# Performance work log

Hardware: AMD Instinct MI355X
Metric: run time of the kernel (lower is better)

Reference implementation:

```python
import jax, jax.numpy as jnp
import numpy as np


def _bicubic_warp(img, dx, dy):
    """Faithful JAX port of Warp_Object.forward with flag='bicubic'.
    img: [B,C,H,W] float32; dx, dy: [B,1,H,W] pixel displacements.
    Replicates the original tile-order quirk: X/Y are repeated C times along
    dim0 (order c*B+b) while the image is flattened in b*C+c order.
    """
    B, C, H, W = img.shape
    Wm1 = jnp.float32(max(W - 1, 1))
    Hm1 = jnp.float32(max(H - 1, 1))
    xs = jnp.arange(W, dtype=jnp.float32)
    ys = jnp.arange(H, dtype=jnp.float32)
    Xg, Yg = jnp.meshgrid(xs, ys)          # [H,W]
    # normalized grid in [-1,1] as in forward()
    newX = 2.0 * (Xg[None] + dx[:, 0]) / Wm1 - 1.0   # [B,H,W]
    newY = 2.0 * (Yg[None] + dy[:, 0]) / Hm1 - 1.0
    # repeat over channels exactly like X.repeat([C,1,1,1]) (tile order)
    x_map = (jnp.tile(newX, (C, 1, 1)) + 1.0) * Wm1 / 2.0   # [B*C,H,W]
    y_map = (jnp.tile(newY, (C, 1, 1)) + 1.0) * Hm1 / 2.0

    x0 = jnp.floor(x_map)
    y0 = jnp.floor(y_map)
    tx = x_map - x0
    ty = y_map - y0

    def cubic_coeffs(t):
        cm1 = (-t ** 3 + 2.0 * t ** 2 - t) / 2.0
        c0 = (3.0 * t ** 3 - 5.0 * t ** 2 + 2.0) / 2.0
        c1 = (-3.0 * t ** 3 + 4.0 * t ** 2 + t) / 2.0
        c2 = 1.0 - (cm1 + c0 + c1)
        return (cm1, c0, c1, c2)

    cx = cubic_coeffs(tx)
    cy = cubic_coeffs(ty)

    x0i = x0.astype(jnp.int32)
    y0i = y0.astype(jnp.int32)
    xi = [jnp.clip(x0i + o, 0, W - 1) for o in (-1, 0, 1, 2)]
    yi = [jnp.clip(y0i + o, 0, H - 1) for o in (-1, 0, 1, 2)]

    flat = img.reshape(B * C, H, W)
    row = jnp.arange(B * C)[:, None, None]   # per-image base offset

    out = jnp.zeros_like(x_map)
    for j in range(4):            # 4 rows of the 4x4 bicubic stencil
        row_acc = jnp.zeros_like(x_map)
        for i in range(4):
            row_acc = row_acc + cx[i] * flat[row, yi[j], xi[i]]
        out = out + cy[j] * row_acc
    return out.reshape(B, C, H, W)


def setup_inputs() -> dict:
    key = jax.random.key(0)
    k1, k2, k3 = jax.random.split(key, 3)
    B, C, H, W = 4, 3, 512, 512
    input_image = jax.random.normal(k1, (B, C, H, W), dtype=jnp.float32)
    delta_x = jax.random.normal(k2, (B, 1, H, W), dtype=jnp.float32) * 1.5
    delta_y = jax.random.normal(k3, (B, 1, H, W), dtype=jnp.float32) * 1.5
    return {"input_image": input_image, "delta_x": delta_x, "delta_y": delta_y}


def reference(input_image, delta_x, delta_y):
    return _bicubic_warp(input_image, delta_x, delta_y)
```

## Files before the change

### kernel.cpp

```cpp
#include <hip/hip_runtime.h>


constexpr int B = 4, C = 3, H = 512, W = 512;
constexpr int HW = H * W;
constexpr int TH = 4;
constexpr int HALO_UP = 6, HALO_DN = 7;
constexpr int RS = TH + HALO_UP + HALO_DN;
constexpr int LST = 272;
constexpr int NPOS = 2;
constexpr int NT = 512;
constexpr int NB = B * (H / TH) * 2;

typedef float f4 __attribute__((ext_vector_type(4)));
typedef f4 f4u __attribute__((aligned(4)));

__global__ __launch_bounds__(NT, 8)
void warp_bicubic_xsplit(const float* __restrict__ img,
                         const float* __restrict__ dxp,
                         const float* __restrict__ dyp,
                         float* __restrict__ out)
{
    __shared__ float tile[RS * LST];

    int b   = blockIdx.x;
    int swz = (b & 7) * (NB / 8) + (b >> 3);
    int bd   = swz >> 8;
    int band = (swz >> 1) & 127;
    int half = swz & 1;
    int yb   = band * TH;
    int xb   = half * 256;
    int cb   = half ? 248 : 0;

    int tid  = threadIdx.x;
    int wave = tid >> 6;
    int ry   = wave >> 1;
    int hw   = wave & 1;
    int lane = tid & 63;
    int y    = yb + ry;
    int xs   = xb + hw * 128 + lane;
    int pixoff = y * W + xs;

    float dxa[NPOS], dya[NPOS];
#pragma unroll
    for (int p = 0; p < NPOS; ++p) {
        dxa[p] = __builtin_nontemporal_load(dxp + bd * HW + pixoff + 64 * p);
        dya[p] = __builtin_nontemporal_load(dyp + bd * HW + pixoff + 64 * p);
    }

    float wx[NPOS][4];
    float cyw[NPOS][4];
    unsigned relv[NPOS];
    unsigned lsv[NPOS];
#pragma unroll
    for (int p = 0; p < NPOS; ++p) {
        int x = xs + 64 * p;
        float xm = (float)x + dxa[p];
        float ym = (float)y + dya[p];
        float x0f = floorf(xm), y0f = floorf(ym);
        float tx = xm - x0f, ty = ym - y0f;
        int x0 = (int)x0f, y0 = (int)y0f;
        int s  = min(max(x0 - 1, 0), W - 4);

        float tx2 = tx * tx, tx3 = tx2 * tx;
        float cx0 = (-tx3 + 2.0f * tx2 - tx) * 0.5f;
        float cx1 = (3.0f * tx3 - 5.0f * tx2 + 2.0f) * 0.5f;
        float cx2 = (-3.0f * tx3 + 4.0f * tx2 + tx) * 0.5f;
        float cx3 = 1.0f - (cx0 + cx1 + cx2);

        float ty2 = ty * ty, ty3 = ty2 * ty;
        cyw[p][0] = (-ty3 + 2.0f * ty2 - ty) * 0.5f;
        cyw[p][1] = (3.0f * ty3 - 5.0f * ty2 + 2.0f) * 0.5f;
        cyw[p][2] = (-3.0f * ty3 + 4.0f * ty2 + ty) * 0.5f;
        cyw[p][3] = 1.0f - (cyw[p][0] + cyw[p][1] + cyw[p][2]);

        if (__builtin_expect(x0 >= 1 && x0 <= W - 3, 1)) {
            wx[p][0] = cx0; wx[p][1] = cx1; wx[p][2] = cx2; wx[p][3] = cx3;
        } else {
            float w0 = 0.f, w1 = 0.f, w2 = 0.f, w3 = 0.f;
            const float cxa[4] = {cx0, cx1, cx2, cx3};
#pragma unroll
            for (int o = 0; o < 4; ++o) {
                int xi = min(max(x0 - 1 + o, 0), W - 1);
                int e  = xi - s;
                float c = cxa[o];
                w0 += (e == 0) ? c : 0.f;
                w1 += (e == 1) ? c : 0.f;
                w2 += (e == 2) ? c : 0.f;
                w3 += (e == 3) ? c : 0.f;
            }
            wx[p][0] = w0; wx[p][1] = w1; wx[p][2] = w2; wx[p][3] = w3;
        }

        relv[p] = (unsigned)(y0 - (yb - HALO_UP + 1));
        lsv[p]  = (unsigned)(s - cb);
    }

#pragma unroll
    for (int c = 0; c < C; ++c) {
        int kp = bd + 4 * c;
        const float* __restrict__ plane = img + (size_t)kp * HW;

        if (c > 0) __syncthreads();
        for (int cc = tid; cc < RS * (LST / 4); cc += NT) {
            int r   = cc / (LST / 4);
            int c4  = (cc - r * (LST / 4)) * 4;
            int scol = min(cb + c4, W - 4);
            int sr   = min(max(yb - HALO_UP + r, 0), H - 1);
            *(f4*)&tile[r * LST + c4] = *(const f4*)(plane + sr * W + scol);
        }
        __syncthreads();

        float* __restrict__ obase = out + (size_t)kp * HW + pixoff;
#pragma unroll
        for (int p = 0; p < NPOS; ++p) {
            float acc;
            if (__builtin_expect(relv[p] <= (unsigned)(RS - 4) &&
                                 lsv[p]  <= (unsigned)(LST - 4), 1)) {
                const float* rp = &tile[relv[p] * LST + lsv[p]];
                float r0 = cyw[p][0] * (wx[p][0]*rp[0] + wx[p][1]*rp[1] + wx[p][2]*rp[2] + wx[p][3]*rp[3]);
                rp += LST;
                float r1 = cyw[p][1] * (wx[p][0]*rp[0] + wx[p][1]*rp[1] + wx[p][2]*rp[2] + wx[p][3]*rp[3]);
                rp += LST;
                float r2 = cyw[p][2] * (wx[p][0]*rp[0] + wx[p][1]*rp[1] + wx[p][2]*rp[2] + wx[p][3]*rp[3]);
                rp += LST;
                float r3 = cyw[p][3] * (wx[p][0]*rp[0] + wx[p][1]*rp[1] + wx[p][2]*rp[2] + wx[p][3]*rp[3]);
                acc = (r0 + r1) + (r2 + r3);
            } else {
                int y0 = (int)relv[p] + (yb - HALO_UP + 1);
                int s  = (int)lsv[p] + cb;
                acc = 0.f;
#pragma unroll
                for (int j = 0; j < 4; ++j) {
                    int yi = min(max(y0 - 1 + j, 0), H - 1);
                    f4 v = *(const f4u*)(plane + yi * W + s);
                    acc += cyw[p][j] * (wx[p][0]*v.x + wx[p][1]*v.y + wx[p][2]*v.z + wx[p][3]*v.w);
                }
            }
            __builtin_nontemporal_store(acc, obase + 64 * p);
        }
    }
}

extern "C" void kernel_launch(void* const* d_in, const int* in_sizes, int n_in,
                              void* d_out, int out_size, void* d_ws, size_t ws_size,
                              hipStream_t stream) {
    const float* img = (const float*)d_in[0];
    const float* dx  = (const float*)d_in[1];
    const float* dy  = (const float*)d_in[2];
    float* out = (float*)d_out;

    dim3 block(NT);
    dim3 grid(NB);
    hipLaunchKernelGGL(warp_bicubic_xsplit, grid, block, 0, stream,
                       img, dx, dy, out);
}
```

Baseline: 17.65 us.

## Double-buffer channel tiles with async global-to-LDS loads and taller bands

Replaces the per-channel load-then-compute tile staging with a double-buffered LDS scheme. It uses global_load_lds to prefetch the next channel's tile while the current channel is interpolated. The band height doubles to 8 rows and the block grows to 1024 threads, which cuts the relative halo overhead and halves the block count. The in-tile test and LDS base offset are also precomputed once per pixel. In exchange the kernel uses twice the LDS per block and relies on correct waitcnt and barrier ordering for the asynchronous LDS writes, and larger blocks may reduce scheduling flexibility.

```diff
diff --git a/kernel.cpp b/kernel.cpp
--- a/kernel.cpp
+++ b/kernel.cpp
@@ -3,29 +3,38 @@
 
 constexpr int B = 4, C = 3, H = 512, W = 512;
 constexpr int HW = H * W;
-constexpr int TH = 4;
+constexpr int TH = 8;
 constexpr int HALO_UP = 6, HALO_DN = 7;
 constexpr int RS = TH + HALO_UP + HALO_DN;
 constexpr int LST = 272;
+constexpr int CH_ROW = LST / 4;
+constexpr int NCHUNK = RS * CH_ROW;
 constexpr int NPOS = 2;
-constexpr int NT = 512;
+constexpr int NT = 1024;
 constexpr int NB = B * (H / TH) * 2;
 
 typedef float f4 __attribute__((ext_vector_type(4)));
 typedef f4 f4u __attribute__((aligned(4)));
 
+typedef const __attribute__((address_space(1))) void* gas_t;
+typedef __attribute__((address_space(3))) void* las_t;
+
+__device__ __forceinline__ void gload_lds16(const float* g, float* l) {
+    __builtin_amdgcn_global_load_lds((gas_t)g, (las_t)l, 16, 0, 0);
+}
+
 __global__ __launch_bounds__(NT, 8)
-void warp_bicubic_xsplit(const float* __restrict__ img,
-                         const float* __restrict__ dxp,
-                         const float* __restrict__ dyp,
-                         float* __restrict__ out)
+void warp_bicubic_dbuf(const float* __restrict__ img,
+                       const float* __restrict__ dxp,
+                       const float* __restrict__ dyp,
+                       float* __restrict__ out)
 {
-    __shared__ float tile[RS * LST];
+    __shared__ float tile[2][RS * LST];
 
     int b   = blockIdx.x;
     int swz = (b & 7) * (NB / 8) + (b >> 3);
-    int bd   = swz >> 8;
-    int band = (swz >> 1) & 127;
+    int bd   = swz >> 7;
+    int band = (swz >> 1) & 63;
     int half = swz & 1;
     int yb   = band * TH;
     int xb   = half * 256;
@@ -40,6 +49,17 @@
     int xs   = xb + hw * 128 + lane;
     int pixoff = y * W + xs;
 
+    {
+        const float* plane = img + (size_t)bd * HW;
+        for (int cc = tid; cc < NCHUNK; cc += NT) {
+            int r  = cc / CH_ROW;
+            int c4 = (cc - r * CH_ROW) * 4;
+            int scol = min(cb + c4, W - 4);
+            int sr   = min(max(yb - HALO_UP + r, 0), H - 1);
+            gload_lds16(plane + sr * W + scol, &tile[0][cc * 4]);
+        }
+    }
+
     float dxa[NPOS], dya[NPOS];
 #pragma unroll
     for (int p = 0; p < NPOS; ++p) {
@@ -49,8 +69,9 @@
 
     float wx[NPOS][4];
     float cyw[NPOS][4];
-    unsigned relv[NPOS];
-    unsigned lsv[NPOS];
+    int   lbase[NPOS];
+    unsigned relv[NPOS], lsv[NPOS];
+    bool  intile[NPOS];
 #pragma unroll
     for (int p = 0; p < NPOS; ++p) {
         int x = xs + 64 * p;
@@ -91,32 +112,37 @@
             wx[p][0] = w0; wx[p][1] = w1; wx[p][2] = w2; wx[p][3] = w3;
         }
 
-        relv[p] = (unsigned)(y0 - (yb - HALO_UP + 1));
-        lsv[p]  = (unsigned)(s - cb);
+        relv[p]  = (unsigned)(y0 - (yb - HALO_UP + 1));
+        lsv[p]   = (unsigned)(s - cb);
+        intile[p] = (relv[p] <= (unsigned)(RS - 4)) & (lsv[p] <= (unsigned)(LST - 4));
+        lbase[p] = (int)relv[p] * LST + (int)lsv[p];
     }
+
+    __syncthreads();
 
 #pragma unroll
     for (int c = 0; c < C; ++c) {
+        int nb = c & 1;
+        if (c + 1 < C) {
+            const float* plane = img + (size_t)(bd + 4 * (c + 1)) * HW;
+            for (int cc = tid; cc < NCHUNK; cc += NT) {
+                int r  = cc / CH_ROW;
+                int c4 = (cc - r * CH_ROW) * 4;
+                int scol = min(cb + c4, W - 4);
+                int sr   = min(max(yb - HALO_UP + r, 0), H - 1);
+                gload_lds16(plane + sr * W + scol, &tile[nb ^ 1][cc * 4]);
+            }
+        }
+
         int kp = bd + 4 * c;
         const float* __restrict__ plane = img + (size_t)kp * HW;
-
-        if (c > 0) __syncthreads();
-        for (int cc = tid; cc < RS * (LST / 4); cc += NT) {
-            int r   = cc / (LST / 4);
-            int c4  = (cc - r * (LST / 4)) * 4;
-            int scol = min(cb + c4, W - 4);
-            int sr   = min(max(yb - HALO_UP + r, 0), H - 1);
-            *(f4*)&tile[r * LST + c4] = *(const f4*)(plane + sr * W + scol);
-        }
-        __syncthreads();
-
+        const float* __restrict__ tp = &tile[nb][0];
         float* __restrict__ obase = out + (size_t)kp * HW + pixoff;
 #pragma unroll
         for (int p = 0; p < NPOS; ++p) {
             float acc;
-            if (__builtin_expect(relv[p] <= (unsigned)(RS - 4) &&
-                                 lsv[p]  <= (unsigned)(LST - 4), 1)) {
-                const float* rp = &tile[relv[p] * LST + lsv[p]];
+            if (__builtin_expect(intile[p], 1)) {
+                const float* rp = tp + lbase[p];
                 float r0 = cyw[p][0] * (wx[p][0]*rp[0] + wx[p][1]*rp[1] + wx[p][2]*rp[2] + wx[p][3]*rp[3]);
                 rp += LST;
                 float r1 = cyw[p][1] * (wx[p][0]*rp[0] + wx[p][1]*rp[1] + wx[p][2]*rp[2] + wx[p][3]*rp[3]);
@@ -138,6 +164,8 @@
             }
             __builtin_nontemporal_store(acc, obase + 64 * p);
         }
+
+        if (c + 1 < C) __syncthreads();
     }
 }
 
@@ -151,6 +179,6 @@
 
     dim3 block(NT);
     dim3 grid(NB);
-    hipLaunchKernelGGL(warp_bicubic_xsplit, grid, block, 0, stream,
+    hipLaunchKernelGGL(warp_bicubic_dbuf, grid, block, 0, stream,
                        img, dx, dy, out);
 }
```

Result: faster. 16.77 us (-5.0%).
